# Kernel optimization log

Hardware: AMD Instinct MI355X
Metric: run time of the kernel (lower is better)

Reference implementation:

```python
import jax, jax.numpy as jnp
import numpy as np

KERNEL_SIZE = 5
PAD = (KERNEL_SIZE - 1) // 2  # ZeroPad2d(2)
MID = PAD
# all 24 kernel offsets except the center (documented intent of the module)
OFFSETS = [(i, j) for i in range(KERNEL_SIZE) for j in range(KERNEL_SIZE)
           if not (i == MID and j == MID)]


def setup_inputs() -> dict:
    key = jax.random.key(0)
    k1, k2, k3 = jax.random.split(key, 3)
    B, C, H, Wd = 16, 1, 512, 512
    OUT = 32
    x = jax.random.normal(k1, (B, C, H, Wd), dtype=jnp.float32)
    # 1x1 conv weight [out_ch, in_ch=24] (squeezed from [out,24,1,1]) and bias
    W = jax.random.normal(k2, (OUT, 24), dtype=jnp.float32) * 0.1
    b = jax.random.normal(k3, (OUT,), dtype=jnp.float32) * 0.1
    return {"x": x, "W": W, "b": b}


def reference(x, W, b):
    B, C, H, Wd = x.shape  # C == 1
    xp = jnp.pad(x, ((0, 0), (0, 0), (PAD, PAD), (PAD, PAD)))
    # shift-subtract: 24 neighbor differences, concatenated on channel dim
    chans = jnp.concatenate(
        [xp[:, :, i:H + i, j:Wd + j] - x for (i, j) in OFFSETS], axis=1
    )  # [B, 24, H, W]
    # 1x1 conv = per-pixel channel mix
    out = jnp.einsum('bchw,oc->bohw', chans, W) + b[None, :, None, None]
    return out
```

## Files before the change

kernel.cpp:

```cpp
#include <hip/hip_runtime.h>


#define H_DIM 512
#define W_DIM 512
#define BATCH 16
#define OUTC 32

#define TILE_W 256
#define TILE_H 4
#define BLOCK_X 64
#define BLOCK_Y 4
#define HALO_W (TILE_W + 4)
#define LDS_W  (TILE_W + 8)
#define LDS_H  (TILE_H + 4)

__global__ __launch_bounds__(64) void pc_prep(const float* __restrict__ W,
                                              float* __restrict__ K) {
    int o = threadIdx.x;
    if (o < OUTC) {
        float s = 0.f;
        #pragma unroll
        for (int c = 0; c < 24; ++c) s += W[o * 24 + c];
        #pragma unroll
        for (int t = 0; t < 25; ++t) {
            float v = (t == 12) ? -s : W[o * 24 + (t < 12 ? t : t - 1)];
            K[o * 25 + t] = v;
        }
    }
}

__global__ __launch_bounds__(256) void pc_conv(const float* __restrict__ x,
                                               const float* __restrict__ K,
                                               const float* __restrict__ bias,
                                               float* __restrict__ out) {
    __shared__ float lds[LDS_H * LDS_W];

    const int b  = blockIdx.z;
    const int h0 = blockIdx.y * TILE_H;
    const int w0 = blockIdx.x * TILE_W;
    const int tx = threadIdx.x;
    const int ty = threadIdx.y;
    const int tid = ty * BLOCK_X + tx;

    const float* xb = x + (size_t)b * H_DIM * W_DIM;

    for (int idx = tid; idx < LDS_H * HALO_W; idx += BLOCK_X * BLOCK_Y) {
        int r = idx / HALO_W;
        int c = idx - r * HALO_W;
        int gh = h0 - 2 + r;
        int gw = w0 - 2 + c;
        float v = 0.f;
        if ((unsigned)gh < (unsigned)H_DIM && (unsigned)gw < (unsigned)W_DIM)
            v = xb[gh * W_DIM + gw];
        lds[r * LDS_W + c] = v;
    }
    __syncthreads();

    float nb[5][8];
    #pragma unroll
    for (int r = 0; r < 5; ++r) {
        const float4* p = (const float4*)&lds[(ty + r) * LDS_W + 4 * tx];
        float4 a = p[0];
        float4 c = p[1];
        nb[r][0] = a.x; nb[r][1] = a.y; nb[r][2] = a.z; nb[r][3] = a.w;
        nb[r][4] = c.x; nb[r][5] = c.y; nb[r][6] = c.z; nb[r][7] = c.w;
    }

    const int h = h0 + ty;
    const int w = w0 + 4 * tx;
    float* op = out + (size_t)b * OUTC * H_DIM * W_DIM + (size_t)h * W_DIM + w;

    #pragma unroll 1
    for (int o = 0; o < OUTC; ++o) {
        const float* kr = K + o * 25;
        float bb = bias[o];
        float acc0 = bb, acc1 = bb, acc2 = bb, acc3 = bb;
        #pragma unroll
        for (int ki = 0; ki < 5; ++ki) {
            #pragma unroll
            for (int kj = 0; kj < 5; ++kj) {
                float k = kr[ki * 5 + kj];
                acc0 += k * nb[ki][kj + 0];
                acc1 += k * nb[ki][kj + 1];
                acc2 += k * nb[ki][kj + 2];
                acc3 += k * nb[ki][kj + 3];
            }
        }
        *(float4*)op = make_float4(acc0, acc1, acc2, acc3);
        op += H_DIM * W_DIM;
    }
}

extern "C" void kernel_launch(void* const* d_in, const int* in_sizes, int n_in,
                              void* d_out, int out_size, void* d_ws, size_t ws_size,
                              hipStream_t stream) {
    const float* x    = (const float*)d_in[0];
    const float* W    = (const float*)d_in[1];
    const float* bias = (const float*)d_in[2];
    float* out = (float*)d_out;
    float* K   = (float*)d_ws;

    pc_prep<<<1, 64, 0, stream>>>(W, K);

    dim3 grid(W_DIM / TILE_W, H_DIM / TILE_H, BATCH);
    dim3 block(BLOCK_X, BLOCK_Y, 1);
    pc_conv<<<grid, block, 0, stream>>>(x, K, bias, out);
}
```

Before: 549.4 us.

## Use full-width row tiles with 8 outputs per thread

Each block now covers the full 512-wide image row over 8 rows, with 512 threads. Each thread computes 8 adjacent output pixels instead of 4. The halo load becomes simple per-row coalesced loads with explicit zero padding at the edges. This cuts the horizontal halo overhead and the redundant neighbor loads per output, at the cost of more registers per thread and fewer, larger blocks. The kernel is output-write bound (32 channels of output), so the gain may be limited.

```diff
diff --git a/kernel.cpp b/kernel.cpp
--- a/kernel.cpp
+++ b/kernel.cpp
@@ -6,13 +6,9 @@
 #define BATCH 16
 #define OUTC 32
 
-#define TILE_W 256
-#define TILE_H 4
-#define BLOCK_X 64
-#define BLOCK_Y 4
-#define HALO_W (TILE_W + 4)
-#define LDS_W  (TILE_W + 8)
-#define LDS_H  (TILE_H + 4)
+#define TILE_H 8
+#define ROWS_STAGE (TILE_H + 4)
+#define LDS_W 520
 
 __global__ __launch_bounds__(64) void pc_prep(const float* __restrict__ W,
                                               float* __restrict__ K) {
@@ -29,64 +25,74 @@
     }
 }
 
-__global__ __launch_bounds__(256) void pc_conv(const float* __restrict__ x,
+__global__ __launch_bounds__(512) void pc_conv(const float* __restrict__ x,
                                                const float* __restrict__ K,
                                                const float* __restrict__ bias,
                                                float* __restrict__ out) {
-    __shared__ float lds[LDS_H * LDS_W];
+    __shared__ float lds[ROWS_STAGE * LDS_W];
 
-    const int b  = blockIdx.z;
-    const int h0 = blockIdx.y * TILE_H;
-    const int w0 = blockIdx.x * TILE_W;
+    const int b  = blockIdx.y;
+    const int h0 = blockIdx.x * TILE_H;
     const int tx = threadIdx.x;
     const int ty = threadIdx.y;
-    const int tid = ty * BLOCK_X + tx;
+    const int tid = ty * 64 + tx;
 
     const float* xb = x + (size_t)b * H_DIM * W_DIM;
 
-    for (int idx = tid; idx < LDS_H * HALO_W; idx += BLOCK_X * BLOCK_Y) {
-        int r = idx / HALO_W;
-        int c = idx - r * HALO_W;
+    #pragma unroll
+    for (int r = 0; r < ROWS_STAGE; ++r) {
         int gh = h0 - 2 + r;
-        int gw = w0 - 2 + c;
         float v = 0.f;
-        if ((unsigned)gh < (unsigned)H_DIM && (unsigned)gw < (unsigned)W_DIM)
-            v = xb[gh * W_DIM + gw];
-        lds[r * LDS_W + c] = v;
+        if ((unsigned)gh < (unsigned)H_DIM) v = xb[gh * W_DIM + tid];
+        lds[r * LDS_W + 2 + tid] = v;
+    }
+    if (tid < ROWS_STAGE * 4) {
+        int r  = tid >> 2;
+        int c4 = tid & 3;
+        int c  = (c4 < 2) ? c4 : (512 + c4);
+        lds[r * LDS_W + c] = 0.f;
     }
     __syncthreads();
 
-    float nb[5][8];
+    float nb[5][12];
     #pragma unroll
     for (int r = 0; r < 5; ++r) {
-        const float4* p = (const float4*)&lds[(ty + r) * LDS_W + 4 * tx];
-        float4 a = p[0];
-        float4 c = p[1];
-        nb[r][0] = a.x; nb[r][1] = a.y; nb[r][2] = a.z; nb[r][3] = a.w;
-        nb[r][4] = c.x; nb[r][5] = c.y; nb[r][6] = c.z; nb[r][7] = c.w;
+        const float* row = &lds[(ty + r) * LDS_W + 8 * tx];
+        float4 a = *(const float4*)(row);
+        float4 m = *(const float4*)(row + 4);
+        float4 c = *(const float4*)(row + 8);
+        nb[r][0] = a.x; nb[r][1]  = a.y; nb[r][2]  = a.z; nb[r][3]  = a.w;
+        nb[r][4] = m.x; nb[r][5]  = m.y; nb[r][6]  = m.z; nb[r][7]  = m.w;
+        nb[r][8] = c.x; nb[r][9]  = c.y; nb[r][10] = c.z; nb[r][11] = c.w;
     }
 
     const int h = h0 + ty;
-    const int w = w0 + 4 * tx;
-    float* op = out + (size_t)b * OUTC * H_DIM * W_DIM + (size_t)h * W_DIM + w;
+    float* op = out + (size_t)b * OUTC * H_DIM * W_DIM
+                    + (size_t)h * W_DIM + 8 * tx;
 
     #pragma unroll 1
     for (int o = 0; o < OUTC; ++o) {
         const float* kr = K + o * 25;
         float bb = bias[o];
-        float acc0 = bb, acc1 = bb, acc2 = bb, acc3 = bb;
+        float a0 = bb, a1 = bb, a2 = bb, a3 = bb;
+        float a4 = bb, a5 = bb, a6 = bb, a7 = bb;
         #pragma unroll
         for (int ki = 0; ki < 5; ++ki) {
             #pragma unroll
             for (int kj = 0; kj < 5; ++kj) {
                 float k = kr[ki * 5 + kj];
-                acc0 += k * nb[ki][kj + 0];
-                acc1 += k * nb[ki][kj + 1];
-                acc2 += k * nb[ki][kj + 2];
-                acc3 += k * nb[ki][kj + 3];
+                a0 += k * nb[ki][kj + 0];
+                a1 += k * nb[ki][kj + 1];
+                a2 += k * nb[ki][kj + 2];
+                a3 += k * nb[ki][kj + 3];
+                a4 += k * nb[ki][kj + 4];
+                a5 += k * nb[ki][kj + 5];
+                a6 += k * nb[ki][kj + 6];
+                a7 += k * nb[ki][kj + 7];
             }
         }
-        *(float4*)op = make_float4(acc0, acc1, acc2, acc3);
+        *(float4*)op       = make_float4(a0, a1, a2, a3);
+        *(float4*)(op + 4) = make_float4(a4, a5, a6, a7);
         op += H_DIM * W_DIM;
     }
 }
@@ -102,7 +108,7 @@
 
     pc_prep<<<1, 64, 0, stream>>>(W, K);
 
-    dim3 grid(W_DIM / TILE_W, H_DIM / TILE_H, BATCH);
-    dim3 block(BLOCK_X, BLOCK_Y, 1);
+    dim3 grid(H_DIM / TILE_H, BATCH, 1);
+    dim3 block(64, TILE_H, 1);
     pc_conv<<<grid, block, 0, stream>>>(x, K, bias, out);
 }
```

Result: no change. 558.7 us (+1.7%).
